# Optimization experiments

Measured on AMD Instinct MI355X. Metric: run time of the kernel, lower is better.

Reference implementation:

```python
import jax, jax.numpy as jnp
import numpy as np

N_NODES = 100000
N_EDGES = 3200000
D = 64          # in == hidden == out channels
EDGE_DIM = 8
N_LAYERS = 3
EPS = 1e-5


def setup_inputs() -> dict:
    key = jax.random.key(0)
    ks = jax.random.split(key, 12)
    x = jax.random.normal(ks[0], (N_NODES, D), dtype=jnp.float32)
    edge_index = jax.random.randint(ks[1], (2, N_EDGES), 0, N_NODES, dtype=jnp.int64)
    edge_attr = jax.random.normal(ks[2], (N_EDGES, EDGE_DIM), dtype=jnp.float32)
    # per-layer HydroConv params (stacked over layers)
    lin_w = jax.random.normal(ks[3], (N_LAYERS, D, D), dtype=jnp.float32) * 0.1
    lin_b = jax.random.normal(ks[4], (N_LAYERS, D), dtype=jnp.float32) * 0.1
    emlp_w = jax.random.normal(ks[5], (N_LAYERS, 1, EDGE_DIM), dtype=jnp.float32) * 0.1
    emlp_b = jax.random.normal(ks[6], (N_LAYERS, 1), dtype=jnp.float32) * 0.1
    # per-layer LayerNorm affine params
    gamma = jnp.ones((N_LAYERS, D), dtype=jnp.float32)
    beta = jnp.zeros((N_LAYERS, D), dtype=jnp.float32)
    fc_w = jax.random.normal(ks[7], (D, D), dtype=jnp.float32) * 0.1
    fc_b = jax.random.normal(ks[8], (D,), dtype=jnp.float32) * 0.1
    return dict(x=x, edge_index=edge_index, edge_attr=edge_attr,
                lin_w=lin_w, lin_b=lin_b, emlp_w=emlp_w, emlp_b=emlp_b,
                gamma=gamma, beta=beta, fc_w=fc_w, fc_b=fc_b)


def _layer_norm(h, g, b):
    mu = jnp.mean(h, axis=-1, keepdims=True)
    var = jnp.var(h, axis=-1, keepdims=True)
    return (h - mu) * jax.lax.rsqrt(var + EPS) * g + b


def reference(x, edge_index, edge_attr, lin_w, lin_b, emlp_w, emlp_b, gamma, beta, fc_w, fc_b):
    src = edge_index[0]  # x_j (source / neighbor)
    dst = edge_index[1]  # x_i (target, aggregation index)
    h = x
    for l in range(N_LAYERS):
        identity = h
        # edge MLP: Linear(edge_dim -> 1) + Softplus  -> per-edge weight [E, 1]
        w = jax.nn.softplus(edge_attr @ emlp_w[l].T + emlp_b[l])
        # message = w * (x_j - x_i); scatter-add to targets
        msg = w * (h[src] - h[dst])                               # [E, D]
        agg = jax.ops.segment_sum(msg, dst, num_segments=N_NODES)  # [N, D]
        h = agg @ lin_w[l].T + lin_b[l]
        h = jax.nn.relu(h)
        h = _layer_norm(h, gamma[l], beta[l])
        h = h + identity  # residual (shapes always match: in == hidden)
    return h @ fc_w.T + fc_b
```

## Files before the change

### kernel.cpp

```cpp
#include <hip/hip_runtime.h>

#define NN 100000
#define NE 3200000
#define NBKT 391
#define NBLK 256
#define EPB (NE / NBLK)
#define GH_N (NBKT * NBLK)

__device__ inline unsigned short f2bf(float f) {
    unsigned int u = __float_as_uint(f);
    u += 0x7FFFu + ((u >> 16) & 1u);
    return (unsigned short)(u >> 16);
}
__device__ inline float bflo(unsigned int v) { return __uint_as_float(v << 16); }
__device__ inline float bfhi(unsigned int v) { return __uint_as_float(v & 0xFFFF0000u); }

__global__ __launch_bounds__(256) void k_transpose(
    const float* __restrict__ linw, const float* __restrict__ fcw,
    float* __restrict__ wt)
{
    const float* src = (blockIdx.x < 3) ? (linw + blockIdx.x * 4096) : fcw;
    float* dst = wt + blockIdx.x * 4096;
    for (int i = threadIdx.x; i < 4096; i += 256)
        dst[(i & 63) * 64 + (i >> 6)] = src[i];
}

__global__ __launch_bounds__(256) void k_cvt(
    const float* __restrict__ x, unsigned short* __restrict__ hb)
{
    int stride = gridDim.x * blockDim.x;
    const float4* x4 = (const float4*)x;
    ushort4* hb4 = (ushort4*)hb;
    for (int i = blockIdx.x * blockDim.x + threadIdx.x; i < NN * 16; i += stride) {
        float4 v = x4[i];
        hb4[i] = make_ushort4(f2bf(v.x), f2bf(v.y), f2bf(v.z), f2bf(v.w));
    }
}

__global__ __launch_bounds__(1024) void k_hist2(
    const int* __restrict__ ei, int* __restrict__ deg, int* __restrict__ gh)
{
    __shared__ int lh[NBKT];
    for (int t = threadIdx.x; t < NBKT; t += 1024) lh[t] = 0;
    __syncthreads();
    int bi = blockIdx.x;
    int e1 = bi * EPB + EPB;
    for (int e = bi * EPB + threadIdx.x; e < e1; e += 1024) {
        int dst = ei[NE + e];
        atomicAdd(&deg[dst], 1);
        atomicAdd(&lh[dst >> 8], 1);
    }
    __syncthreads();
    for (int t = threadIdx.x; t < NBKT; t += 1024)
        gh[t * NBLK + bi] = lh[t];
}

__global__ __launch_bounds__(256) void k_scan1(
    const int* __restrict__ in, int* __restrict__ out, int* __restrict__ csum, int n)
{
    __shared__ int lds[256];
    int tid = threadIdx.x;
    int i0 = blockIdx.x * 1024 + tid * 4;
    int d[4];
    #pragma unroll
    for (int k = 0; k < 4; ++k) d[k] = (i0 + k < n) ? in[i0 + k] : 0;
    int s = d[0] + d[1] + d[2] + d[3];
    lds[tid] = s;
    __syncthreads();
    for (int off = 1; off < 256; off <<= 1) {
        int add = (tid >= off) ? lds[tid - off] : 0;
        __syncthreads();
        lds[tid] += add;
        __syncthreads();
    }
    int excl = lds[tid] - s;
    if (i0 + 0 < n) out[i0 + 0] = excl;
    if (i0 + 1 < n) out[i0 + 1] = excl + d[0];
    if (i0 + 2 < n) out[i0 + 2] = excl + d[0] + d[1];
    if (i0 + 3 < n) out[i0 + 3] = excl + d[0] + d[1] + d[2];
    if (tid == 255) csum[blockIdx.x] = lds[255];
}

__global__ __launch_bounds__(128) void k_scan2(
    const int* __restrict__ csum, int* __restrict__ coff, int nchunk)
{
    __shared__ int lds[128];
    int tid = threadIdx.x;
    int v = (tid < nchunk) ? csum[tid] : 0;
    lds[tid] = v;
    __syncthreads();
    for (int off = 1; off < 128; off <<= 1) {
        int add = (tid >= off) ? lds[tid - off] : 0;
        __syncthreads();
        lds[tid] += add;
        __syncthreads();
    }
    coff[tid] = lds[tid] - v;
}

__global__ __launch_bounds__(256) void k_scan3(
    int* __restrict__ arr, const int* __restrict__ coff, int n)
{
    int off = coff[blockIdx.x];
    int i0 = blockIdx.x * 1024 + threadIdx.x * 4;
    #pragma unroll
    for (int k = 0; k < 4; ++k)
        if (i0 + k < n) arr[i0 + k] += off;
    if (blockIdx.x == 0 && threadIdx.x == 0) arr[n] = NE;
}

__global__ __launch_bounds__(1024) void k_fill(
    const int* __restrict__ ei, const float* __restrict__ ea,
    const float* __restrict__ mw, const float* __restrict__ mb,
    const int* __restrict__ goff, uint2* __restrict__ stg,
    unsigned char* __restrict__ stgd)
{
    __shared__ int lcur[NBKT];
    int bi = blockIdx.x;
    for (int t = threadIdx.x; t < NBKT; t += 1024) lcur[t] = goff[t * NBLK + bi];
    __syncthreads();
    float wl[3][8], bl[3];
    #pragma unroll
    for (int l = 0; l < 3; ++l) {
        bl[l] = mb[l];
        #pragma unroll
        for (int k = 0; k < 8; ++k) wl[l][k] = mw[l * 8 + k];
    }
    const float4* ea4 = (const float4*)ea;
    int e1 = bi * EPB + EPB;
    for (int e = bi * EPB + threadIdx.x; e < e1; e += 1024) {
        float4 a0 = ea4[2 * e], a1 = ea4[2 * e + 1];
        float av[8] = {a0.x, a0.y, a0.z, a0.w, a1.x, a1.y, a1.z, a1.w};
        unsigned int wb[3];
        #pragma unroll
        for (int l = 0; l < 3; ++l) {
            float xx = bl[l];
            #pragma unroll
            for (int k = 0; k < 8; ++k) xx += av[k] * wl[l][k];
            float sp = fmaxf(xx, 0.f) + log1pf(expf(-fabsf(xx)));
            wb[l] = f2bf(sp) & 0x7FFFu;
        }
        int src = ei[e], dst = ei[NE + e];
        int slot = atomicAdd(&lcur[dst >> 8], 1);
        uint2 rec;
        rec.x = (unsigned int)src | (wb[0] << 17);
        rec.y = wb[1] | (wb[2] << 15);
        stg[slot] = rec;
        stgd[slot] = (unsigned char)(dst & 255);
    }
}

__global__ __launch_bounds__(256) void k_fill2(
    const int* __restrict__ base, const uint2* __restrict__ stg,
    const unsigned char* __restrict__ stgd, uint2* __restrict__ pk)
{
    __shared__ int bl[256];
    __shared__ int cnt[256];
    int b = blockIdx.x;
    int n0 = b * 256;
    int t = threadIdx.x;
    if (n0 + t < NN) { bl[t] = base[n0 + t]; }
    cnt[t] = 0;
    __syncthreads();
    int s0 = base[n0];
    int s1 = (n0 + 256 <= NN) ? base[n0 + 256] : NE;
    for (int s = s0 + t; s < s1; s += 256) {
        uint2 rec = stg[s];
        int dl = stgd[s];
        int r = atomicAdd(&cnt[dl], 1);
        pk[bl[dl] + r] = rec;
    }
}

template<int L>
__device__ inline float dec_w(uint2 p) {
    if (L == 0) return __uint_as_float((p.x >> 17) << 16);
    if (L == 1) return __uint_as_float((p.y & 0x7FFFu) << 16);
    return __uint_as_float((p.y >> 15) << 16);
}

template<int L>
__global__ __launch_bounds__(256) void k_agg(
    const int* __restrict__ base, const uint2* __restrict__ pk,
    const unsigned short* __restrict__ hb, const float* __restrict__ h,
    float* __restrict__ aout)
{
    int lane = threadIdx.x & 63;
    int sub = lane & 7;
    int g = lane >> 3;
    int wid = (blockIdx.x * blockDim.x + threadIdx.x) >> 6;
    int nwave = (gridDim.x * blockDim.x) >> 6;
    for (int n = wid * 8 + g; n < NN; n += nwave * 8) {
        int s = base[n], e2 = base[n + 1];
        float a0 = 0.f, a1 = 0.f, a2 = 0.f, a3 = 0.f;
        float a4 = 0.f, a5 = 0.f, a6 = 0.f, a7 = 0.f, wsn = 0.f;
        int sl = s;
        for (; sl + 4 <= e2; sl += 4) {
            uint2 p0 = pk[sl], p1 = pk[sl + 1], p2 = pk[sl + 2], p3 = pk[sl + 3];
            uint4 v0 = *(const uint4*)(hb + (((size_t)(p0.x & 0x1FFFF)) << 6) + (sub << 3));
            uint4 v1 = *(const uint4*)(hb + (((size_t)(p1.x & 0x1FFFF)) << 6) + (sub << 3));
            uint4 v2 = *(const uint4*)(hb + (((size_t)(p2.x & 0x1FFFF)) << 6) + (sub << 3));
            uint4 v3 = *(const uint4*)(hb + (((size_t)(p3.x & 0x1FFFF)) << 6) + (sub << 3));
            float w0 = dec_w<L>(p0), w1 = dec_w<L>(p1), w2 = dec_w<L>(p2), w3 = dec_w<L>(p3);
            a0 += w0 * bflo(v0.x); a1 += w0 * bfhi(v0.x); a2 += w0 * bflo(v0.y); a3 += w0 * bfhi(v0.y);
            a4 += w0 * bflo(v0.z); a5 += w0 * bfhi(v0.z); a6 += w0 * bflo(v0.w); a7 += w0 * bfhi(v0.w);
            a0 += w1 * bflo(v1.x); a1 += w1 * bfhi(v1.x); a2 += w1 * bflo(v1.y); a3 += w1 * bfhi(v1.y);
            a4 += w1 * bflo(v1.z); a5 += w1 * bfhi(v1.z); a6 += w1 * bflo(v1.w); a7 += w1 * bfhi(v1.w);
            a0 += w2 * bflo(v2.x); a1 += w2 * bfhi(v2.x); a2 += w2 * bflo(v2.y); a3 += w2 * bfhi(v2.y);
            a4 += w2 * bflo(v2.z); a5 += w2 * bfhi(v2.z); a6 += w2 * bflo(v2.w); a7 += w2 * bfhi(v2.w);
            a0 += w3 * bflo(v3.x); a1 += w3 * bfhi(v3.x); a2 += w3 * bflo(v3.y); a3 += w3 * bfhi(v3.y);
            a4 += w3 * bflo(v3.z); a5 += w3 * bfhi(v3.z); a6 += w3 * bflo(v3.w); a7 += w3 * bfhi(v3.w);
            wsn += w0 + w1 + w2 + w3;
        }
        for (; sl < e2; ++sl) {
            uint2 p = pk[sl];
            uint4 v = *(const uint4*)(hb + (((size_t)(p.x & 0x1FFFF)) << 6) + (sub << 3));
            float w = dec_w<L>(p);
            a0 += w * bflo(v.x); a1 += w * bfhi(v.x); a2 += w * bflo(v.y); a3 += w * bfhi(v.y);
            a4 += w * bflo(v.z); a5 += w * bfhi(v.z); a6 += w * bflo(v.w); a7 += w * bfhi(v.w);
            wsn += w;
        }
        const float* hrow = h + (size_t)n * 64 + sub * 8;
        float4 h0 = *(const float4*)hrow;
        float4 h1 = *(const float4*)(hrow + 4);
        float* orow = aout + (size_t)n * 64 + sub * 8;
        float4 o0 = {a0 - wsn * h0.x, a1 - wsn * h0.y, a2 - wsn * h0.z, a3 - wsn * h0.w};
        float4 o1 = {a4 - wsn * h1.x, a5 - wsn * h1.y, a6 - wsn * h1.z, a7 - wsn * h1.w};
        *(float4*)orow = o0;
        *(float4*)(orow + 4) = o1;
    }
}

__global__ __launch_bounds__(256) void k_node(
    const float* a, const float* __restrict__ hin, float* hout,
    unsigned short* __restrict__ hbout,
    const float* __restrict__ wt, const float* __restrict__ bias,
    const float* __restrict__ gamma, const float* __restrict__ beta)
{
    int n0 = blockIdx.x * blockDim.x + threadIdx.x;
    int stride = gridDim.x * blockDim.x;
    const float4* a4 = (const float4*)a;
    const float4* hin4 = (const float4*)hin;
    float4* ho4 = (float4*)hout;
    ushort4* hb4 = (ushort4*)hbout;
    for (int n = n0; n < NN; n += stride) {
        float y[64];
        #pragma unroll
        for (int j = 0; j < 64; ++j) y[j] = bias[j];
        #pragma unroll 2
        for (int k4 = 0; k4 < 16; ++k4) {
            float4 gg = a4[n * 16 + k4];
            float av[4] = {gg.x, gg.y, gg.z, gg.w};
            #pragma unroll
            for (int kk = 0; kk < 4; ++kk) {
                const float* wr = wt + (k4 * 4 + kk) * 64;
                #pragma unroll
                for (int j = 0; j < 64; ++j) y[j] += av[kk] * wr[j];
            }
        }
        float s = 0.f, s2 = 0.f;
        #pragma unroll
        for (int j = 0; j < 64; ++j) {
            y[j] = fmaxf(y[j], 0.f);
            s += y[j]; s2 += y[j] * y[j];
        }
        float mu = s * (1.f / 64.f);
        float var = s2 * (1.f / 64.f) - mu * mu;
        float inv = rsqrtf(var + 1e-5f);
        #pragma unroll
        for (int j4 = 0; j4 < 16; ++j4) {
            float4 hh = hin4[n * 16 + j4];
            float4 o;
            o.x = (y[4*j4+0] - mu) * inv * gamma[4*j4+0] + beta[4*j4+0] + hh.x;
            o.y = (y[4*j4+1] - mu) * inv * gamma[4*j4+1] + beta[4*j4+1] + hh.y;
            o.z = (y[4*j4+2] - mu) * inv * gamma[4*j4+2] + beta[4*j4+2] + hh.z;
            o.w = (y[4*j4+3] - mu) * inv * gamma[4*j4+3] + beta[4*j4+3] + hh.w;
            ho4[n * 16 + j4] = o;
            if (hbout)
                hb4[n * 16 + j4] = make_ushort4(f2bf(o.x), f2bf(o.y), f2bf(o.z), f2bf(o.w));
        }
    }
}

__global__ __launch_bounds__(256) void k_fc(
    const float* __restrict__ hin, float* __restrict__ out,
    const float* __restrict__ wt, const float* __restrict__ bias)
{
    int n0 = blockIdx.x * blockDim.x + threadIdx.x;
    int stride = gridDim.x * blockDim.x;
    const float4* hin4 = (const float4*)hin;
    float4* o4 = (float4*)out;
    for (int n = n0; n < NN; n += stride) {
        float y[64];
        #pragma unroll
        for (int j = 0; j < 64; ++j) y[j] = bias[j];
        #pragma unroll 2
        for (int k4 = 0; k4 < 16; ++k4) {
            float4 hh = hin4[n * 16 + k4];
            float hv[4] = {hh.x, hh.y, hh.z, hh.w};
            #pragma unroll
            for (int kk = 0; kk < 4; ++kk) {
                const float* wr = wt + (k4 * 4 + kk) * 64;
                #pragma unroll
                for (int j = 0; j < 64; ++j) y[j] += hv[kk] * wr[j];
            }
        }
        #pragma unroll
        for (int j4 = 0; j4 < 16; ++j4) {
            float4 o = {y[4*j4], y[4*j4+1], y[4*j4+2], y[4*j4+3]};
            o4[n * 16 + j4] = o;
        }
    }
}

extern "C" void kernel_launch(void* const* d_in, const int* in_sizes, int n_in,
                              void* d_out, int out_size, void* d_ws, size_t ws_size,
                              hipStream_t stream)
{
    const float* x     = (const float*)d_in[0];
    const int*   ei    = (const int*)d_in[1];
    const float* ea    = (const float*)d_in[2];
    const float* linw  = (const float*)d_in[3];
    const float* linb  = (const float*)d_in[4];
    const float* mw    = (const float*)d_in[5];
    const float* mb    = (const float*)d_in[6];
    const float* gamma = (const float*)d_in[7];
    const float* beta  = (const float*)d_in[8];
    const float* fcw   = (const float*)d_in[9];
    const float* fcb   = (const float*)d_in[10];
    float* out = (float*)d_out;

    float*  A    = (float*)d_ws;
    float*  C    = A + (size_t)NN * 64;
    uint2*  pk   = (uint2*)(C + (size_t)NN * 64);
    unsigned short* hb = (unsigned short*)(pk + NE);
    float*  wt   = (float*)(hb + (size_t)NN * 64);
    int*    deg  = (int*)(wt + 4 * 4096);
    int*    base = deg + NN;
    int*    gh   = base + NN + 1;
    int*    goff = gh + GH_N;
    int*    csum = goff + GH_N + 1;
    int*    coff = csum + 128;
    uint2*  stg  = (uint2*)C;
    unsigned char* stgd = (unsigned char*)A;

    k_transpose<<<4, 256, 0, stream>>>(linw, fcw, wt);
    k_cvt<<<2048, 256, 0, stream>>>(x, hb);
    hipMemsetAsync(deg, 0, NN * sizeof(int), stream);
    k_hist2<<<NBLK, 1024, 0, stream>>>(ei, deg, gh);
    k_scan1<<<98, 256, 0, stream>>>(deg, base, csum, NN);
    k_scan2<<<1, 128, 0, stream>>>(csum, coff, 98);
    k_scan3<<<98, 256, 0, stream>>>(base, coff, NN);
    k_scan1<<<98, 256, 0, stream>>>(gh, goff, csum, GH_N);
    k_scan2<<<1, 128, 0, stream>>>(csum, coff, 98);
    k_scan3<<<98, 256, 0, stream>>>(goff, coff, GH_N);
    k_fill<<<NBLK, 1024, 0, stream>>>(ei, ea, mw, mb, goff, stg, stgd);
    k_fill2<<<NBKT, 256, 0, stream>>>(base, stg, stgd, pk);

    k_agg<0><<<3125, 256, 0, stream>>>(base, pk, hb, x, C);
    k_node<<<512, 256, 0, stream>>>(C, x, C, hb, wt + 0 * 4096, linb + 0 * 64,
                                    gamma + 0 * 64, beta + 0 * 64);
    k_agg<1><<<3125, 256, 0, stream>>>(base, pk, hb, C, A);
    k_node<<<512, 256, 0, stream>>>(A, C, A, hb, wt + 1 * 4096, linb + 1 * 64,
                                    gamma + 1 * 64, beta + 1 * 64);
    k_agg<2><<<3125, 256, 0, stream>>>(base, pk, hb, A, C);
    k_node<<<512, 256, 0, stream>>>(C, A, C, (unsigned short*)nullptr,
                                    wt + 2 * 4096, linb + 2 * 64,
                                    gamma + 2 * 64, beta + 2 * 64);

    k_fc<<<512, 256, 0, stream>>>(C, out, wt + 3 * 4096, fcb);
}
```

Before: 878.4 us.

## Derive per-node CSR offsets inside bucket fill instead of global degree pass

Removes the global per-node degree histogram (3.2M global atomics), its memset and the three-kernel node-level scan. Each bucket block in the second fill pass now counts its 256 destination nodes in LDS, runs a local prefix scan offset by the bucket's global start, writes the CSR base array, and scatters records. This cuts global atomic traffic and four launches, at the cost of an extra read pass over the staged destination bytes in the fill kernel.

```diff
diff --git a/kernel.cpp b/kernel.cpp
--- a/kernel.cpp
+++ b/kernel.cpp
@@ -38,18 +38,15 @@
 }
 
 __global__ __launch_bounds__(1024) void k_hist2(
-    const int* __restrict__ ei, int* __restrict__ deg, int* __restrict__ gh)
+    const int* __restrict__ ei, int* __restrict__ gh)
 {
     __shared__ int lh[NBKT];
     for (int t = threadIdx.x; t < NBKT; t += 1024) lh[t] = 0;
     __syncthreads();
     int bi = blockIdx.x;
     int e1 = bi * EPB + EPB;
-    for (int e = bi * EPB + threadIdx.x; e < e1; e += 1024) {
-        int dst = ei[NE + e];
-        atomicAdd(&deg[dst], 1);
-        atomicAdd(&lh[dst >> 8], 1);
-    }
+    for (int e = bi * EPB + threadIdx.x; e < e1; e += 1024)
+        atomicAdd(&lh[ei[NE + e] >> 8], 1);
     __syncthreads();
     for (int t = threadIdx.x; t < NBKT; t += 1024)
         gh[t * NBLK + bi] = lh[t];
@@ -151,24 +148,42 @@
 }
 
 __global__ __launch_bounds__(256) void k_fill2(
-    const int* __restrict__ base, const uint2* __restrict__ stg,
-    const unsigned char* __restrict__ stgd, uint2* __restrict__ pk)
-{
-    __shared__ int bl[256];
+    const int* __restrict__ goff, const uint2* __restrict__ stg,
+    const unsigned char* __restrict__ stgd, uint2* __restrict__ pk,
+    int* __restrict__ base)
+{
     __shared__ int cnt[256];
+    __shared__ int lds[256];
+    __shared__ int pos[256];
     int b = blockIdx.x;
     int n0 = b * 256;
     int t = threadIdx.x;
-    if (n0 + t < NN) { bl[t] = base[n0 + t]; }
+    int s0 = goff[b * NBLK];
+    int s1 = goff[(b + 1) * NBLK];
     cnt[t] = 0;
     __syncthreads();
-    int s0 = base[n0];
-    int s1 = (n0 + 256 <= NN) ? base[n0 + 256] : NE;
+    for (int s = s0 + t; s < s1; s += 256)
+        atomicAdd(&cnt[stgd[s]], 1);
+    __syncthreads();
+    int v = cnt[t];
+    lds[t] = v;
+    __syncthreads();
+    for (int off = 1; off < 256; off <<= 1) {
+        int add = (t >= off) ? lds[t - off] : 0;
+        __syncthreads();
+        lds[t] += add;
+        __syncthreads();
+    }
+    int start = s0 + lds[t] - v;
+    pos[t] = start;
+    if (n0 + t < NN) base[n0 + t] = start;
+    if (b == 0 && t == 0) base[NN] = NE;
+    __syncthreads();
     for (int s = s0 + t; s < s1; s += 256) {
         uint2 rec = stg[s];
         int dl = stgd[s];
-        int r = atomicAdd(&cnt[dl], 1);
-        pk[bl[dl] + r] = rec;
+        int r = atomicAdd(&pos[dl], 1);
+        pk[r] = rec;
     }
 }
 
@@ -335,8 +350,7 @@
     uint2*  pk   = (uint2*)(C + (size_t)NN * 64);
     unsigned short* hb = (unsigned short*)(pk + NE);
     float*  wt   = (float*)(hb + (size_t)NN * 64);
-    int*    deg  = (int*)(wt + 4 * 4096);
-    int*    base = deg + NN;
+    int*    base = (int*)(wt + 4 * 4096);
     int*    gh   = base + NN + 1;
     int*    goff = gh + GH_N;
     int*    csum = goff + GH_N + 1;
@@ -346,16 +360,12 @@
 
     k_transpose<<<4, 256, 0, stream>>>(linw, fcw, wt);
     k_cvt<<<2048, 256, 0, stream>>>(x, hb);
-    hipMemsetAsync(deg, 0, NN * sizeof(int), stream);
-    k_hist2<<<NBLK, 1024, 0, stream>>>(ei, deg, gh);
-    k_scan1<<<98, 256, 0, stream>>>(deg, base, csum, NN);
-    k_scan2<<<1, 128, 0, stream>>>(csum, coff, 98);
-    k_scan3<<<98, 256, 0, stream>>>(base, coff, NN);
+    k_hist2<<<NBLK, 1024, 0, stream>>>(ei, gh);
     k_scan1<<<98, 256, 0, stream>>>(gh, goff, csum, GH_N);
     k_scan2<<<1, 128, 0, stream>>>(csum, coff, 98);
     k_scan3<<<98, 256, 0, stream>>>(goff, coff, GH_N);
     k_fill<<<NBLK, 1024, 0, stream>>>(ei, ea, mw, mb, goff, stg, stgd);
-    k_fill2<<<NBKT, 256, 0, stream>>>(base, stg, stgd, pk);
+    k_fill2<<<NBKT, 256, 0, stream>>>(goff, stg, stgd, pk, base);
 
     k_agg<0><<<3125, 256, 0, stream>>>(base, pk, hb, x, C);
     k_node<<<512, 256, 0, stream>>>(C, x, C, hb, wt + 0 * 4096, linb + 0 * 64,
```

Result: faster. 756.7 us (-13.9%).
